# Kernel tuning notes

Measured on AMD Instinct MI355X. Metric: run time of the kernel, lower is better.

The kernel has to match this reference:

```python
import jax, jax.numpy as jnp
import numpy as np

B, S, E, H, L, F = 64, 256, 480, 6, 8, 1920
D = E // H  # 80
VOCAB, MEL, CHORD = 4833, 257, 4833 - 257
EPS = 1e-5


def setup_inputs() -> dict:
    key = jax.random.key(0)
    ks = jax.random.split(key, 24)
    mel = jax.random.randint(ks[0], (B, S), 0, MEL)
    chd = MEL + jax.random.randint(ks[1], (B, S), 0, CHORD)
    pos = jnp.arange(S) % 2  # 0=melody, 1=chord
    input_tokens = jnp.where(pos[None, :] == 1, chd, mel)
    std = 0.02
    n = lambda k, shp: std * jax.random.normal(k, shp, dtype=jnp.float32)
    return {
        'input_tokens': input_tokens,
        'tok_emb': n(ks[2], (VOCAB, E)),
        'pos_emb': n(ks[3], (S, E)),
        'Wq': n(ks[4], (L, E, E)), 'bq': jnp.zeros((L, E)),
        'Wk': n(ks[5], (L, E, E)), 'bk': jnp.zeros((L, E)),
        'Wv': n(ks[6], (L, E, E)), 'bv': jnp.zeros((L, E)),
        'Wo': n(ks[7], (L, E, E)), 'bo': jnp.zeros((L, E)),
        'ln1_s': jnp.ones((L, E)), 'ln1_b': jnp.zeros((L, E)),
        'ln2_s': jnp.ones((L, E)), 'ln2_b': jnp.zeros((L, E)),
        'W1': n(ks[8], (L, F, E)), 'b1': jnp.zeros((L, F)),
        'W2': n(ks[9], (L, E, F)), 'b2': jnp.zeros((L, E)),
        'Wh': n(ks[10], (CHORD, E)), 'bh': jnp.zeros((CHORD,)),
    }


def _ln(x, s, b):
    mu = jnp.mean(x, -1, keepdims=True)
    var = jnp.var(x, -1, keepdims=True)
    return (x - mu) * jax.lax.rsqrt(var + EPS) * s + b


def reference(input_tokens, tok_emb, pos_emb, Wq, bq, Wk, bk, Wv, bv, Wo, bo,
              ln1_s, ln1_b, ln2_s, ln2_b, W1, b1, W2, b2, Wh, bh):
    x = tok_emb[input_tokens] + pos_emb[None, :, :]  # [B,S,E]
    causal = jnp.tril(jnp.ones((S, S), dtype=bool))  # True = keep
    scale = 1.0 / jnp.sqrt(jnp.float32(D))
    for i in range(L):
        h = _ln(x, ln1_s[i], ln1_b[i])
        q = (h @ Wq[i].T + bq[i]).reshape(B, S, H, D).transpose(0, 2, 1, 3)
        k = (h @ Wk[i].T + bk[i]).reshape(B, S, H, D).transpose(0, 2, 1, 3)
        v = (h @ Wv[i].T + bv[i]).reshape(B, S, H, D).transpose(0, 2, 1, 3)
        scores = jnp.einsum('bhsd,bhtd->bhst', q, k) * scale
        scores = jnp.where(causal[None, None], scores, -jnp.inf)
        attn = jax.nn.softmax(scores, axis=-1)
        o = jnp.einsum('bhst,bhtd->bhsd', attn, v)
        o = o.transpose(0, 2, 1, 3).reshape(B, S, E)
        x = x + (o @ Wo[i].T + bo[i])
        h2 = _ln(x, ln2_s[i], ln2_b[i])
        ff = jax.nn.gelu(h2 @ W1[i].T + b1[i], approximate=False) @ W2[i].T + b2[i]
        x = x + ff
    chord = x[:, 1::2, :]  # [B, S//2, E]
    return chord @ Wh.T + bh
```

## Files before the change

kernel.cpp:

```cpp
#include <hip/hip_runtime.h>
#include <hip/hip_bf16.h>
#include <math.h>

#define B_ 64
#define S_ 256
#define E_ 480
#define H_ 6
#define D_ 80
#define L_ 8
#define F_ 1920
#define CHORD_ 4576
#define TOKENS_ (B_*S_)
#define CROWS_ (B_*128)

typedef unsigned short u16;
typedef unsigned int u32;
typedef unsigned long long u64;
typedef __attribute__((ext_vector_type(8))) short short8;
typedef __attribute__((ext_vector_type(4))) float f32x4;
typedef __attribute__((ext_vector_type(4))) u32 u32x4;

__device__ __forceinline__ float bf_lo(u32 u){ return __uint_as_float(u << 16); }
__device__ __forceinline__ float bf_hi(u32 u){ return __uint_as_float(u & 0xffff0000u); }
__device__ __forceinline__ u16 f2bf(float f){
  u32 u = __float_as_uint(f);
  return (u16)((u + 0x7fffu + ((u >> 16) & 1u)) >> 16);
}

__device__ __forceinline__ void async_cp16(void* lds, const void* g){
  __builtin_amdgcn_global_load_lds((const __attribute__((address_space(1))) void*)g,
                                   (__attribute__((address_space(3))) void*)lds, 16, 0, 0);
}

__global__ void cvt_kernel(const float* __restrict__ s, u16* __restrict__ d, int n4)
{
  int i = blockIdx.x * 256 + threadIdx.x;
  const int stride = gridDim.x * 256;
  for (; i < n4; i += stride){
    float4 v = ((const float4*)s)[i];
    u64 w = (u64)((u32)f2bf(v.x) | ((u32)f2bf(v.y) << 16))
          | ((u64)((u32)f2bf(v.z) | ((u32)f2bf(v.w) << 16)) << 32);
    ((u64*)d)[i] = w;
  }
}

__global__ void embed_kernel(const int* __restrict__ tok,
                             const float* __restrict__ tok_emb,
                             const float* __restrict__ pos_emb,
                             float* __restrict__ x)
{
  int row = blockIdx.x;
  int s = row & (S_-1);
  int t = tok[row];
  const float* te = tok_emb + (size_t)t * E_;
  const float* pe = pos_emb + (size_t)s * E_;
  float* xr = x + (size_t)row * E_;
  for (int e = threadIdx.x; e < E_; e += blockDim.x)
    xr[e] = te[e] + pe[e];
}

__global__ __launch_bounds__(256) void ln_kernel(const float* __restrict__ x,
    const float* __restrict__ g, const float* __restrict__ b, u16* __restrict__ o)
{
  int wid = threadIdx.x >> 6, lane = threadIdx.x & 63;
  int row = blockIdx.x * 4 + wid;
  const float* xr = x + (size_t)row * E_;
  float v[8];
  #pragma unroll
  for (int i = 0; i < 7; ++i) v[i] = xr[lane + i*64];
  v[7] = (lane < 32) ? xr[448 + lane] : 0.f;
  float sum = 0.f, sq = 0.f;
  #pragma unroll
  for (int i = 0; i < 8; ++i){ sum += v[i]; sq += v[i]*v[i]; }
  #pragma unroll
  for (int m = 1; m < 64; m <<= 1){ sum += __shfl_xor(sum, m); sq += __shfl_xor(sq, m); }
  float mean = sum * (1.f/E_);
  float var  = sq  * (1.f/E_) - mean*mean;
  float rs = rsqrtf(var + 1e-5f);
  u16* orow = o + (size_t)row * E_;
  #pragma unroll
  for (int i = 0; i < 7; ++i){
    int idx = lane + i*64;
    orow[idx] = f2bf((v[i]-mean)*rs*g[idx] + b[idx]);
  }
  if (lane < 32){
    int idx = 448 + lane;
    orow[idx] = f2bf((v[7]-mean)*rs*g[idx] + b[idx]);
  }
}

template<int MODE>
__global__ __launch_bounds__(256, 4) void gemm_bf_kernel(const u16* __restrict__ A,
                            const u16* __restrict__ Wb, const float* __restrict__ bias,
                            u16* __restrict__ Cb, float* __restrict__ Cf,
                            int M, int N, int K)
{
  __shared__ u16 As[2][128*32];
  __shared__ u16 Ws[2][128*32];
  const int tid = threadIdx.x;
  const int wid = tid >> 6, lane = tid & 63;
  const int wr = wid >> 1, wc = wid & 1;
  const int lr = lane & 15, kg = lane >> 4;
  const int kgs = kg ^ (lr & 3);
  const int m0 = blockIdx.y * 128;
  const int n0 = blockIdx.x * 128;

  const f32x4 zero = {0.f,0.f,0.f,0.f};
  f32x4 acc[4][4];
  #pragma unroll
  for (int i=0;i<4;i++)
    #pragma unroll
    for (int j=0;j<4;j++)
      acc[i][j] = zero;

  const int srow = tid >> 2;
  const int schunk = (tid & 3) ^ (srow & 3);
  const u16* ap0 = A + (size_t)(m0 + srow) * K + schunk*8;
  const u16* ap1 = ap0 + (size_t)64 * K;
  int r0 = n0 + srow, r1 = r0 + 64;
  if (r0 >= N) r0 = N-1;
  if (r1 >= N) r1 = N-1;
  const u16* wp0 = Wb + (size_t)r0 * K + schunk*8;
  const u16* wp1 = Wb + (size_t)r1 * K + schunk*8;

  #define STAGE(bb, k0) do { \
    char* ab = (char*)As[bb] + wid*1024; \
    char* wb_ = (char*)Ws[bb] + wid*1024; \
    async_cp16(ab,        ap0 + (k0)); \
    async_cp16(ab + 4096, ap1 + (k0)); \
    async_cp16(wb_,        wp0 + (k0)); \
    async_cp16(wb_ + 4096, wp1 + (k0)); \
  } while(0)

  const int nsteps = K >> 5;
  STAGE(0, 0);
  __syncthreads();
  int cur = 0;
  for (int ks = 0; ks < nsteps; ++ks){
    if (ks + 1 < nsteps) STAGE(cur^1, (ks+1) << 5);

    short8 af[4], wf[4];
    #pragma unroll
    for (int i=0;i<4;i++) af[i] = *(const short8*)&As[cur][(wr*64 + i*16 + lr)*32 + kgs*8];
    #pragma unroll
    for (int j=0;j<4;j++) wf[j] = *(const short8*)&Ws[cur][(wc*64 + j*16 + lr)*32 + kgs*8];
    #pragma unroll
    for (int i=0;i<4;i++)
      #pragma unroll
      for (int j=0;j<4;j++)
        acc[i][j] = __builtin_amdgcn_mfma_f32_16x16x32_bf16(af[i], wf[j], acc[i][j], 0, 0, 0);

    __syncthreads();
    cur ^= 1;
  }
  #undef STAGE

  #pragma unroll
  for (int i=0;i<4;i++){
    const int row = m0 + wr*64 + i*16 + kg*4;
    #pragma unroll
    for (int j=0;j<4;j++){
      const int col = n0 + wc*64 + j*16 + lr;
      if (col < N){
        const float bv = bias[col];
        #pragma unroll
        for (int q=0;q<4;q++){
          float val = acc[i][j][q] + bv;
          size_t off = (size_t)(row + q) * N + col;
          if (MODE == 0){
            Cb[off] = f2bf(val);
          } else if (MODE == 1){
            float gx = 0.5f * val * (1.f + erff(val * 0.70710678118654752f));
            Cb[off] = f2bf(gx);
          } else if (MODE == 2){
            Cf[off] += val;
          } else {
            Cf[off] = val;
          }
        }
      }
    }
  }
}

template<int MODE>
__global__ __launch_bounds__(256) void gemm_kernel(const u16* __restrict__ A, const float* __restrict__ W,
                            const float* __restrict__ bias,
                            u16* __restrict__ Cb, float* __restrict__ Cf,
                            int M, int N, int K)
{
  __shared__ u16 As[128*32];
  __shared__ u16 Ws[128*32];
  const int tid = threadIdx.x;
  const int wid = tid >> 6, lane = tid & 63;
  const int wr = wid >> 1, wc = wid & 1;
  const int lr = lane & 15, kg = lane >> 4;
  const int m0 = blockIdx.y * 128;
  const int n0 = blockIdx.x * 128;

  const f32x4 zero = {0.f,0.f,0.f,0.f};
  f32x4 acc[4][4];
  #pragma unroll
  for (int i=0;i<4;i++)
    #pragma unroll
    for (int j=0;j<4;j++)
      acc[i][j] = zero;

  const int trow = tid >> 1;
  const int tcol = (tid & 1) * 16;
  const int wn = n0 + trow;
  const bool wok = wn < N;
  const float* wp = W + (size_t)wn * K + tcol;

  const u16* ap0 = A + (size_t)(m0 + (tid>>2)) * K + (tid&3)*8;
  const u16* ap1 = ap0 + (size_t)64 * K;
  char* lb0 = (char*)As + wid*1024;
  char* lb1 = (char*)As + 4096 + wid*1024;
  u32* wdst = (u32*)&Ws[trow*32 + tcol];

  const int nsteps = K >> 5;
  for (int ks = 0; ks < nsteps; ++ks){
    const int k0 = ks << 5;
    async_cp16(lb0, ap0 + k0);
    async_cp16(lb1, ap1 + k0);

    float wv[16];
    if (wok){
      const float4* s4 = (const float4*)(wp + k0);
      #pragma unroll
      for (int i=0;i<4;i++){
        float4 t4 = s4[i];
        wv[4*i]=t4.x; wv[4*i+1]=t4.y; wv[4*i+2]=t4.z; wv[4*i+3]=t4.w;
      }
    } else {
      #pragma unroll
      for (int i=0;i<16;i++) wv[i]=0.f;
    }
    u32 pk[8];
    #pragma unroll
    for (int i=0;i<8;i++) pk[i] = (u32)f2bf(wv[2*i]) | ((u32)f2bf(wv[2*i+1]) << 16);
    #pragma unroll
    for (int i=0;i<8;i++) wdst[i] = pk[i];

    __syncthreads();

    short8 af[4], wf[4];
    #pragma unroll
    for (int i=0;i<4;i++) af[i] = *(const short8*)&As[(wr*64 + i*16 + lr)*32 + kg*8];
    #pragma unroll
    for (int j=0;j<4;j++) wf[j] = *(const short8*)&Ws[(wc*64 + j*16 + lr)*32 + kg*8];
    #pragma unroll
    for (int i=0;i<4;i++)
      #pragma unroll
      for (int j=0;j<4;j++)
        acc[i][j] = __builtin_amdgcn_mfma_f32_16x16x32_bf16(af[i], wf[j], acc[i][j], 0, 0, 0);

    __syncthreads();
  }

  #pragma unroll
  for (int i=0;i<4;i++){
    const int row = m0 + wr*64 + i*16 + kg*4;
    #pragma unroll
    for (int j=0;j<4;j++){
      const int col = n0 + wc*64 + j*16 + lr;
      if (col < N){
        const float bv = bias[col];
        #pragma unroll
        for (int q=0;q<4;q++){
          float val = acc[i][j][q] + bv;
          size_t off = (size_t)(row + q) * N + col;
          if (MODE == 0){
            Cb[off] = f2bf(val);
          } else if (MODE == 1){
            float gx = 0.5f * val * (1.f + erff(val * 0.70710678118654752f));
            Cb[off] = f2bf(gx);
          } else if (MODE == 2){
            Cf[off] += val;
          } else {
            Cf[off] = val;
          }
        }
      }
    }
  }
}

#define KSTRIDE 104
#define VSTRIDE 264
__global__ __launch_bounds__(256) void attn_mfma_kernel(const u16* __restrict__ Q,
    const u16* __restrict__ K, const u16* __restrict__ V, u16* __restrict__ O)
{
  __shared__ u16 ks[256*KSTRIDE];
  __shared__ u16 vt[80*VSTRIDE];
  const int bh = blockIdx.x;
  const int b = bh / H_, h = bh - b*H_;
  const int tid = threadIdx.x;
  const int wv = tid >> 6, lane = tid & 63;
  const int q16 = lane & 15, g = lane >> 4;
  const size_t base = (size_t)b * S_ * E_ + h * D_;

  {
    const uint4* kr = (const uint4*)(K + base + (size_t)tid * E_);
    uint4 t0[10];
    #pragma unroll
    for (int i=0;i<10;i++) t0[i] = kr[i];
    u16* krow = &ks[tid*KSTRIDE];
    #pragma unroll
    for (int i=0;i<10;i++) *(uint4*)&krow[i*8] = t0[i];
    const uint4 z4 = {0,0,0,0};
    *(uint4*)&krow[80] = z4;
    *(uint4*)&krow[88] = z4;
  }
  {
    const u32* vr = (const u32*)(V + base + (size_t)tid * E_);
    u32 t1[40];
    #pragma unroll
    for (int i=0;i<40;i++) t1[i] = vr[i];
    #pragma unroll
    for (int i=0;i<40;i++){
      vt[(2*i)*VSTRIDE + tid]   = (u16)(t1[i] & 0xffffu);
      vt[(2*i+1)*VSTRIDE + tid] = (u16)(t1[i] >> 16);
    }
  }
  short8 bq[4][3];
  const short8 z8 = {0,0,0,0,0,0,0,0};
  #pragma unroll
  for (int i=0;i<4;i++){
    const int qr = 16*wv + 64*i;
    const u16* qrow = Q + (size_t)(b*S_ + qr + q16) * E_ + h*D_;
    bq[i][0] = *(const short8*)&qrow[g*8];
    bq[i][1] = *(const short8*)&qrow[32 + g*8];
    bq[i][2] = (g < 2) ? *(const short8*)&qrow[64 + g*8] : z8;
  }
  __syncthreads();

  f32x4 o_[4][5];
  float m_[4], l_[4];
  #pragma unroll
  for (int i=0;i<4;i++){
    m_[i] = -1e30f; l_[i] = 0.f;
    #pragma unroll
    for (int j=0;j<5;j++) o_[i][j] = (f32x4){0.f,0.f,0.f,0.f};
  }
  const float scale = 0.1118033988749895f;
  const int ktmaxw = (16*wv + 207) >> 5;

  for (int kt = 0; kt <= ktmaxw; ++kt){
    short8 af[2][3];
    #pragma unroll
    for (int a=0;a<2;a++)
      #pragma unroll
      for (int kk=0;kk<3;kk++)
        af[a][kk] = *(const short8*)&ks[(32*kt + 16*a + q16)*KSTRIDE + kk*32 + g*8];
    short8 bvv[5];
    #pragma unroll
    for (int j=0;j<5;j++)
      bvv[j] = *(const short8*)&vt[(16*j + q16)*VSTRIDE + kt*32 + g*8];

    #pragma unroll
    for (int i=0;i<4;i++){
      const int qr = 16*wv + 64*i;
      if (kt > ((qr + 15) >> 5)) continue;
      f32x4 c0 = {0.f,0.f,0.f,0.f}, c1 = {0.f,0.f,0.f,0.f};
      #pragma unroll
      for (int kk=0;kk<3;kk++){
        c0 = __builtin_amdgcn_mfma_f32_16x16x32_bf16(af[0][kk], bq[i][kk], c0, 0, 0, 0);
        c1 = __builtin_amdgcn_mfma_f32_16x16x32_bf16(af[1][kk], bq[i][kk], c1, 0, 0, 0);
      }
      const int qglob = qr + q16;
      const int kb0 = 32*kt + 4*g;
      const bool diag = (32*kt + 31) > qr;
      float s0[4], s1[4];
      #pragma unroll
      for (int r=0;r<4;r++){
        s0[r] = c0[r] * scale;
        s1[r] = c1[r] * scale;
        if (diag){
          if (kb0 + r > qglob)      s0[r] = -3e38f;
          if (kb0 + 16 + r > qglob) s1[r] = -3e38f;
        }
      }
      float mx = fmaxf(fmaxf(fmaxf(s0[0],s0[1]),fmaxf(s0[2],s0[3])),
                       fmaxf(fmaxf(s1[0],s1[1]),fmaxf(s1[2],s1[3])));
      mx = fmaxf(mx, __shfl_xor(mx, 16));
      mx = fmaxf(mx, __shfl_xor(mx, 32));
      const float mnew = fmaxf(m_[i], mx);
      const float resc = __expf(m_[i] - mnew);
      float p0[4], p1[4], ps = 0.f;
      #pragma unroll
      for (int r=0;r<4;r++){
        p0[r] = __expf(s0[r] - mnew);
        p1[r] = __expf(s1[r] - mnew);
        ps += p0[r] + p1[r];
      }
      ps += __shfl_xor(ps, 16);
      ps += __shfl_xor(ps, 32);
      l_[i] = l_[i] * resc + ps;
      m_[i] = mnew;
      float fr[4];
      #pragma unroll
      for (int r=0;r<4;r++) fr[r] = __shfl(resc, 4*g + r);
      #pragma unroll
      for (int j=0;j<5;j++){
        #pragma unroll
        for (int r=0;r<4;r++) o_[i][j][r] *= fr[r];
      }
      u32 pw0 = (u32)f2bf(p0[0]) | ((u32)f2bf(p0[1]) << 16);
      u32 pw1 = (u32)f2bf(p0[2]) | ((u32)f2bf(p0[3]) << 16);
      u32 pw2 = (u32)f2bf(p1[0]) | ((u32)f2bf(p1[1]) << 16);
      u32 pw3 = (u32)f2bf(p1[2]) | ((u32)f2bf(p1[3]) << 16);
      const int s01 = ((((g<<1)&3)<<4) + q16) << 2;
      const int s23 = (((((g<<1)+1)&3)<<4) + q16) << 2;
      int rA0 = __builtin_amdgcn_ds_bpermute(s01, (int)pw0);
      int rB0 = __builtin_amdgcn_ds_bpermute(s01, (int)pw2);
      int rA1 = __builtin_amdgcn_ds_bpermute(s01, (int)pw1);
      int rB1 = __builtin_amdgcn_ds_bpermute(s01, (int)pw3);
      int rA2 = __builtin_amdgcn_ds_bpermute(s23, (int)pw0);
      int rB2 = __builtin_amdgcn_ds_bpermute(s23, (int)pw2);
      int rA3 = __builtin_amdgcn_ds_bpermute(s23, (int)pw1);
      int rB3 = __builtin_amdgcn_ds_bpermute(s23, (int)pw3);
      const bool lo = (g < 2);
      u32x4 rw = { (u32)(lo ? rA0 : rB0), (u32)(lo ? rA1 : rB1),
                   (u32)(lo ? rA2 : rB2), (u32)(lo ? rA3 : rB3) };
      short8 pa = __builtin_bit_cast(short8, rw);
      #pragma unroll
      for (int j=0;j<5;j++)
        o_[i][j] = __builtin_amdgcn_mfma_f32_16x16x32_bf16(pa, bvv[j], o_[i][j], 0, 0, 0);
    }
  }

  #pragma unroll
  for (int i=0;i<4;i++){
    const int qr = 16*wv + 64*i;
    const float inv = 1.f / l_[i];
    float fr[4];
    #pragma unroll
    for (int r=0;r<4;r++) fr[r] = __shfl(inv, 4*g + r);
    #pragma unroll
    for (int j=0;j<5;j++){
      #pragma unroll
      for (int r=0;r<4;r++){
        const int row = qr + 4*g + r;
        O[(size_t)(b*S_ + row) * E_ + h*D_ + 16*j + q16] = f2bf(o_[i][j][r] * fr[r]);
      }
    }
  }
}

__global__ void gather_kernel(const float* __restrict__ x, u16* __restrict__ cin)
{
  int i = blockIdx.x * 256 + threadIdx.x;
  if (i >= CROWS_*E_) return;
  int row = i / E_, col = i - row*E_;
  int b = row >> 7, r = row & 127;
  cin[i] = f2bf(x[((size_t)(b*S_ + 2*r + 1))*E_ + col]);
}

extern "C" void kernel_launch(void* const* d_in, const int* in_sizes, int n_in,
                              void* d_out, int out_size, void* d_ws, size_t ws_size,
                              hipStream_t stream)
{
  (void)in_sizes; (void)n_in; (void)out_size;
  const int*   tok     = (const int*)d_in[0];
  const float* tok_emb = (const float*)d_in[1];
  const float* pos_emb = (const float*)d_in[2];
  const float* Wq = (const float*)d_in[3];
  const float* bq = (const float*)d_in[4];
  const float* Wk = (const float*)d_in[5];
  const float* bk = (const float*)d_in[6];
  const float* Wv = (const float*)d_in[7];
  const float* bv = (const float*)d_in[8];
  const float* Wo = (const float*)d_in[9];
  const float* bo = (const float*)d_in[10];
  const float* ln1s = (const float*)d_in[11];
  const float* ln1b = (const float*)d_in[12];
  const float* ln2s = (const float*)d_in[13];
  const float* ln2b = (const float*)d_in[14];
  const float* W1 = (const float*)d_in[15];
  const float* b1 = (const float*)d_in[16];
  const float* W2 = (const float*)d_in[17];
  const float* b2 = (const float*)d_in[18];
  const float* Wh = (const float*)d_in[19];
  const float* bh = (const float*)d_in[20];

  char* p = (char*)d_ws;
  float* x  = (float*)p;            p += (size_t)TOKENS_*E_*4;
  u16* h    = (u16*)p;              p += (size_t)TOKENS_*E_*2;
  u16* qb   = (u16*)p;
  u16* kb   = qb + (size_t)TOKENS_*E_;
  u16* vb   = kb + (size_t)TOKENS_*E_;
  u16* ao   = vb + (size_t)TOKENS_*E_;
  u16* ff1  = qb;
  u16* cin  = h;
  p += (size_t)4*TOKENS_*E_*2;

  const size_t szE  = (size_t)L_*E_*E_;
  const size_t szF  = (size_t)L_*F_*E_;
  const size_t szH  = (size_t)CHORD_*E_;
  u16* wq_bf = (u16*)p;
  u16* wk_bf = wq_bf + szE;
  u16* wv_bf = wk_bf + szE;
  u16* wo_bf = wv_bf + szE;
  u16* w1_bf = wo_bf + szE;
  u16* w2_bf = w1_bf + szF;
  u16* wh_bf = w2_bf + szF;
  const size_t need = (size_t)110100480 + 2*(4*szE + 2*szF + szH);
  const bool bf16w = (ws_size >= need);

  embed_kernel<<<TOKENS_, 128, 0, stream>>>(tok, tok_emb, pos_emb, x);

  dim3 blk(256);
  dim3 gE(4, TOKENS_/128);
  dim3 gF1(15, TOKENS_/128);
  dim3 gHd(36, CROWS_/128);

  if (bf16w){
    cvt_kernel<<<1024, blk, 0, stream>>>(Wq, wq_bf, (int)(szE/4));
    cvt_kernel<<<1024, blk, 0, stream>>>(Wk, wk_bf, (int)(szE/4));
    cvt_kernel<<<1024, blk, 0, stream>>>(Wv, wv_bf, (int)(szE/4));
    cvt_kernel<<<1024, blk, 0, stream>>>(Wo, wo_bf, (int)(szE/4));
    cvt_kernel<<<1024, blk, 0, stream>>>(W1, w1_bf, (int)(szF/4));
    cvt_kernel<<<1024, blk, 0, stream>>>(W2, w2_bf, (int)(szF/4));
    cvt_kernel<<<1024, blk, 0, stream>>>(Wh, wh_bf, (int)(szH/4));
    for (int i = 0; i < L_; ++i){
      ln_kernel<<<TOKENS_/4, blk, 0, stream>>>(x, ln1s + i*E_, ln1b + i*E_, h);
      gemm_bf_kernel<0><<<gE, blk, 0, stream>>>(h, wq_bf + (size_t)i*E_*E_, bq + i*E_, qb, nullptr, TOKENS_, E_, E_);
      gemm_bf_kernel<0><<<gE, blk, 0, stream>>>(h, wk_bf + (size_t)i*E_*E_, bk + i*E_, kb, nullptr, TOKENS_, E_, E_);
      gemm_bf_kernel<0><<<gE, blk, 0, stream>>>(h, wv_bf + (size_t)i*E_*E_, bv + i*E_, vb, nullptr, TOKENS_, E_, E_);
      attn_mfma_kernel<<<B_*H_, blk, 0, stream>>>(qb, kb, vb, ao);
      gemm_bf_kernel<2><<<gE, blk, 0, stream>>>(ao, wo_bf + (size_t)i*E_*E_, bo + i*E_, nullptr, x, TOKENS_, E_, E_);
      ln_kernel<<<TOKENS_/4, blk, 0, stream>>>(x, ln2s + i*E_, ln2b + i*E_, h);
      gemm_bf_kernel<1><<<gF1, blk, 0, stream>>>(h, w1_bf + (size_t)i*F_*E_, b1 + i*F_, ff1, nullptr, TOKENS_, F_, E_);
      gemm_bf_kernel<2><<<gE, blk, 0, stream>>>(ff1, w2_bf + (size_t)i*E_*F_, b2 + i*E_, nullptr, x, TOKENS_, E_, F_);
    }
    gather_kernel<<<(CROWS_*E_ + 255)/256, blk, 0, stream>>>(x, cin);
    gemm_bf_kernel<3><<<gHd, blk, 0, stream>>>(cin, wh_bf, bh, nullptr, (float*)d_out, CROWS_, CHORD_, E_);
  } else {
    for (int i = 0; i < L_; ++i){
      ln_kernel<<<TOKENS_/4, blk, 0, stream>>>(x, ln1s + i*E_, ln1b + i*E_, h);
      gemm_kernel<0><<<gE, blk, 0, stream>>>(h, Wq + (size_t)i*E_*E_, bq + i*E_, qb, nullptr, TOKENS_, E_, E_);
      gemm_kernel<0><<<gE, blk, 0, stream>>>(h, Wk + (size_t)i*E_*E_, bk + i*E_, kb, nullptr, TOKENS_, E_, E_);
      gemm_kernel<0><<<gE, blk, 0, stream>>>(h, Wv + (size_t)i*E_*E_, bv + i*E_, vb, nullptr, TOKENS_, E_, E_);
      attn_mfma_kernel<<<B_*H_, blk, 0, stream>>>(qb, kb, vb, ao);
      gemm_kernel<2><<<gE, blk, 0, stream>>>(ao, Wo + (size_t)i*E_*E_, bo + i*E_, nullptr, x, TOKENS_, E_, E_);
      ln_kernel<<<TOKENS_/4, blk, 0, stream>>>(x, ln2s + i*E_, ln2b + i*E_, h);
      gemm_kernel<1><<<gF1, blk, 0, stream>>>(h, W1 + (size_t)i*F_*E_, b1 + i*F_, ff1, nullptr, TOKENS_, F_, E_);
      gemm_kernel<2><<<gE, blk, 0, stream>>>(ff1, W2 + (size_t)i*E_*F_, b2 + i*E_, nullptr, x, TOKENS_, E_, F_);
    }
    gather_kernel<<<(CROWS_*E_ + 255)/256, blk, 0, stream>>>(x, cin);
    gemm_kernel<3><<<gHd, blk, 0, stream>>>(cin, Wh, bh, nullptr, (float*)d_out, CROWS_, CHORD_, E_);
  }
}
```

Baseline: 2.412 ms.

## Fuse Q/K/V projections into one GEMM and add XCD-aware tile remapping

```diff
diff --git a/kernel.cpp b/kernel.cpp
--- a/kernel.cpp
+++ b/kernel.cpp
@@ -12,6 +12,7 @@
 #define CHORD_ 4576
 #define TOKENS_ (B_*S_)
 #define CROWS_ (B_*128)
+#define QS_ 1440
 
 typedef unsigned short u16;
 typedef unsigned int u32;
@@ -20,8 +21,6 @@
 typedef __attribute__((ext_vector_type(4))) float f32x4;
 typedef __attribute__((ext_vector_type(4))) u32 u32x4;
 
-__device__ __forceinline__ float bf_lo(u32 u){ return __uint_as_float(u << 16); }
-__device__ __forceinline__ float bf_hi(u32 u){ return __uint_as_float(u & 0xffff0000u); }
 __device__ __forceinline__ u16 f2bf(float f){
   u32 u = __float_as_uint(f);
   return (u16)((u + 0x7fffu + ((u >> 16) & 1u)) >> 16);
@@ -30,6 +29,16 @@
 __device__ __forceinline__ void async_cp16(void* lds, const void* g){
   __builtin_amdgcn_global_load_lds((const __attribute__((address_space(1))) void*)g,
                                    (__attribute__((address_space(3))) void*)lds, 16, 0, 0);
+}
+
+__device__ __forceinline__ void xcd_tile(int gx, int gy, int& tx, int& ty){
+  const int nwg = gx * gy;
+  const int bid = blockIdx.y * gx + blockIdx.x;
+  const int xcd = bid & 7, slot = bid >> 3;
+  const int q8 = nwg >> 3, r8 = nwg & 7;
+  const int t = slot + (xcd < r8 ? xcd * (q8 + 1) : r8 * (q8 + 1) + (xcd - r8) * q8);
+  ty = t / gx;
+  tx = t - ty * gx;
 }
 
 __global__ void cvt_kernel(const float* __restrict__ s, u16* __restrict__ d, int n4)
@@ -42,6 +51,36 @@
           | ((u64)((u32)f2bf(v.z) | ((u32)f2bf(v.w) << 16)) << 32);
     ((u64*)d)[i] = w;
   }
+}
+
+__global__ void qkv_cvt_kernel(const float* __restrict__ Wq, const float* __restrict__ Wk,
+                               const float* __restrict__ Wv, u16* __restrict__ dst)
+{
+  const int per = E_*E_/4;
+  const int tot = L_*3*per;
+  int i = blockIdx.x * 256 + threadIdx.x;
+  const int stride = gridDim.x * 256;
+  for (; i < tot; i += stride){
+    int l = i / (3*per);
+    int rem = i - l*3*per;
+    int sel = rem / per;
+    int r2 = rem - sel*per;
+    const float* src = (sel == 0) ? Wq : (sel == 1) ? Wk : Wv;
+    float4 v = ((const float4*)(src + (size_t)l*E_*E_))[r2];
+    u64 w = (u64)((u32)f2bf(v.x) | ((u32)f2bf(v.y) << 16))
+          | ((u64)((u32)f2bf(v.z) | ((u32)f2bf(v.w) << 16)) << 32);
+    ((u64*)dst)[i] = w;
+  }
+}
+
+__global__ void bias_cat_kernel(const float* __restrict__ bq, const float* __restrict__ bk,
+                                const float* __restrict__ bv, float* __restrict__ dst)
+{
+  int i = blockIdx.x * 256 + threadIdx.x;
+  if (i >= L_*QS_) return;
+  int l = i / QS_, c = i - l*QS_;
+  float v = (c < 480) ? bq[l*480 + c] : (c < 960) ? bk[l*480 + c - 480] : bv[l*480 + c - 960];
+  dst[i] = v;
 }
 
 __global__ void embed_kernel(const int* __restrict__ tok,
@@ -93,7 +132,7 @@
 __global__ __launch_bounds__(256, 4) void gemm_bf_kernel(const u16* __restrict__ A,
                             const u16* __restrict__ Wb, const float* __restrict__ bias,
                             u16* __restrict__ Cb, float* __restrict__ Cf,
-                            int M, int N, int K)
+                            int M, int N, int K, int ldc)
 {
   __shared__ u16 As[2][128*32];
   __shared__ u16 Ws[2][128*32];
@@ -102,8 +141,10 @@
   const int wr = wid >> 1, wc = wid & 1;
   const int lr = lane & 15, kg = lane >> 4;
   const int kgs = kg ^ (lr & 3);
-  const int m0 = blockIdx.y * 128;
-  const int n0 = blockIdx.x * 128;
+  int tx, ty;
+  xcd_tile(gridDim.x, gridDim.y, tx, ty);
+  const int m0 = ty * 128;
+  const int n0 = tx * 128;
 
   const f32x4 zero = {0.f,0.f,0.f,0.f};
   f32x4 acc[4][4];
@@ -166,7 +207,7 @@
         #pragma unroll
         for (int q=0;q<4;q++){
           float val = acc[i][j][q] + bv;
-          size_t off = (size_t)(row + q) * N + col;
+          size_t off = (size_t)(row + q) * ldc + col;
           if (MODE == 0){
             Cb[off] = f2bf(val);
           } else if (MODE == 1){
@@ -187,7 +228,7 @@
 __global__ __launch_bounds__(256) void gemm_kernel(const u16* __restrict__ A, const float* __restrict__ W,
                             const float* __restrict__ bias,
                             u16* __restrict__ Cb, float* __restrict__ Cf,
-                            int M, int N, int K)
+                            int M, int N, int K, int ldc)
 {
   __shared__ u16 As[128*32];
   __shared__ u16 Ws[128*32];
@@ -195,8 +236,10 @@
   const int wid = tid >> 6, lane = tid & 63;
   const int wr = wid >> 1, wc = wid & 1;
   const int lr = lane & 15, kg = lane >> 4;
-  const int m0 = blockIdx.y * 128;
-  const int n0 = blockIdx.x * 128;
+  int tx, ty;
+  xcd_tile(gridDim.x, gridDim.y, tx, ty);
+  const int m0 = ty * 128;
+  const int n0 = tx * 128;
 
   const f32x4 zero = {0.f,0.f,0.f,0.f};
   f32x4 acc[4][4];
@@ -269,7 +312,7 @@
         #pragma unroll
         for (int q=0;q<4;q++){
           float val = acc[i][j][q] + bv;
-          size_t off = (size_t)(row + q) * N + col;
+          size_t off = (size_t)(row + q) * ldc + col;
           if (MODE == 0){
             Cb[off] = f2bf(val);
           } else if (MODE == 1){
@@ -288,8 +331,8 @@
 
 #define KSTRIDE 104
 #define VSTRIDE 264
-__global__ __launch_bounds__(256) void attn_mfma_kernel(const u16* __restrict__ Q,
-    const u16* __restrict__ K, const u16* __restrict__ V, u16* __restrict__ O)
+__global__ __launch_bounds__(256) void attn_mfma_kernel(const u16* __restrict__ QKV,
+                                                        u16* __restrict__ O)
 {
   __shared__ u16 ks[256*KSTRIDE];
   __shared__ u16 vt[80*VSTRIDE];
@@ -298,10 +341,10 @@
   const int tid = threadIdx.x;
   const int wv = tid >> 6, lane = tid & 63;
   const int q16 = lane & 15, g = lane >> 4;
-  const size_t base = (size_t)b * S_ * E_ + h * D_;
+  const size_t rowbase = (size_t)(b*S_ + tid) * QS_ + h * D_;
 
   {
-    const uint4* kr = (const uint4*)(K + base + (size_t)tid * E_);
+    const uint4* kr = (const uint4*)(QKV + rowbase + 480);
     uint4 t0[10];
     #pragma unroll
     for (int i=0;i<10;i++) t0[i] = kr[i];
@@ -313,7 +356,7 @@
     *(uint4*)&krow[88] = z4;
   }
   {
-    const u32* vr = (const u32*)(V + base + (size_t)tid * E_);
+    const u32* vr = (const u32*)(QKV + rowbase + 960);
     u32 t1[40];
     #pragma unroll
     for (int i=0;i<40;i++) t1[i] = vr[i];
@@ -328,7 +371,7 @@
   #pragma unroll
   for (int i=0;i<4;i++){
     const int qr = 16*wv + 64*i;
-    const u16* qrow = Q + (size_t)(b*S_ + qr + q16) * E_ + h*D_;
+    const u16* qrow = QKV + (size_t)(b*S_ + qr + q16) * QS_ + h*D_;
     bq[i][0] = *(const short8*)&qrow[g*8];
     bq[i][1] = *(const short8*)&qrow[32 + g*8];
     bq[i][2] = (g < 2) ? *(const short8*)&qrow[64 + g*8] : z8;
@@ -487,68 +530,63 @@
   char* p = (char*)d_ws;
   float* x  = (float*)p;            p += (size_t)TOKENS_*E_*4;
   u16* h    = (u16*)p;              p += (size_t)TOKENS_*E_*2;
-  u16* qb   = (u16*)p;
-  u16* kb   = qb + (size_t)TOKENS_*E_;
-  u16* vb   = kb + (size_t)TOKENS_*E_;
-  u16* ao   = vb + (size_t)TOKENS_*E_;
-  u16* ff1  = qb;
+  u16* qkv  = (u16*)p;
+  u16* ao   = qkv + (size_t)TOKENS_*QS_;
+  u16* ff1  = qkv;
   u16* cin  = h;
-  p += (size_t)4*TOKENS_*E_*2;
+  p += (size_t)TOKENS_*QS_*2 + (size_t)TOKENS_*E_*2;
 
   const size_t szE  = (size_t)L_*E_*E_;
   const size_t szF  = (size_t)L_*F_*E_;
   const size_t szH  = (size_t)CHORD_*E_;
-  u16* wq_bf = (u16*)p;
-  u16* wk_bf = wq_bf + szE;
-  u16* wv_bf = wk_bf + szE;
-  u16* wo_bf = wv_bf + szE;
-  u16* w1_bf = wo_bf + szE;
-  u16* w2_bf = w1_bf + szF;
-  u16* wh_bf = w2_bf + szF;
-  const size_t need = (size_t)110100480 + 2*(4*szE + 2*szF + szH);
+  u16* wqkv_bf = (u16*)p;            p += 3*szE*2;
+  u16* wo_bf   = (u16*)p;            p += szE*2;
+  u16* w1_bf   = (u16*)p;            p += szF*2;
+  u16* w2_bf   = (u16*)p;            p += szF*2;
+  u16* wh_bf   = (u16*)p;            p += szH*2;
+  float* bqkv  = (float*)p;          p += (size_t)L_*QS_*4;
+  const size_t need = (size_t)(p - (char*)d_ws);
   const bool bf16w = (ws_size >= need);
 
   embed_kernel<<<TOKENS_, 128, 0, stream>>>(tok, tok_emb, pos_emb, x);
 
   dim3 blk(256);
+  dim3 gQKV(12, TOKENS_/128);
   dim3 gE(4, TOKENS_/128);
   dim3 gF1(15, TOKENS_/128);
   dim3 gHd(36, CROWS_/128);
 
   if (bf16w){
-    cvt_kernel<<<1024, blk, 0, stream>>>(Wq, wq_bf, (int)(szE/4));
-    cvt_kernel<<<1024, blk, 0, stream>>>(Wk, wk_bf, (int)(szE/4));
-    cvt_kernel<<<1024, blk, 0, stream>>>(Wv, wv_bf, (int)(szE/4));
+    qkv_cvt_kernel<<<2048, blk, 0, stream>>>(Wq, Wk, Wv, wqkv_bf);
+    bias_cat_kernel<<<(L_*QS_ + 255)/256, blk, 0, stream>>>(bq, bk, bv, bqkv);
     cvt_kernel<<<1024, blk, 0, stream>>>(Wo, wo_bf, (int)(szE/4));
     cvt_kernel<<<1024, blk, 0, stream>>>(W1, w1_bf, (int)(szF/4));
     cvt_kernel<<<1024, blk, 0, stream>>>(W2, w2_bf, (int)(szF/4));
     cvt_kernel<<<1024, blk, 0, stream>>>(Wh, wh_bf, (int)(szH/4));
     for (int i = 0; i < L_; ++i){
       ln_kernel<<<TOKENS_/4, blk, 0, stream>>>(x, ln1s + i*E_, ln1b + i*E_, h);
-      gemm_bf_kernel<0><<<gE, blk, 0, stream>>>(h, wq_bf + (size_t)i*E_*E_, bq + i*E_, qb, nullptr, TOKENS_, E_, E_);
-      gemm_bf_kernel<0><<<gE, blk, 0, stream>>>(h, wk_bf + (size_t)i*E_*E_, bk + i*E_, kb, nullptr, TOKENS_, E_, E_);
-      gemm_bf_kernel<0><<<gE, blk, 0, stream>>>(h, wv_bf + (size_t)i*E_*E_, bv + i*E_, vb, nullptr, TOKENS_, E_, E_);
-      attn_mfma_kernel<<<B_*H_, blk, 0, stream>>>(qb, kb, vb, ao);
-      gemm_bf_kernel<2><<<gE, blk, 0, stream>>>(ao, wo_bf + (size_t)i*E_*E_, bo + i*E_, nullptr, x, TOKENS_, E_, E_);
+      gemm_bf_kernel<0><<<gQKV, blk, 0, stream>>>(h, wqkv_bf + (size_t)i*3*E_*E_, bqkv + i*QS_, qkv, nullptr, TOKENS_, QS_, E_, QS_);
+      attn_mfma_kernel<<<B_*H_, blk, 0, stream>>>(qkv, ao);
+      gemm_bf_kernel<2><<<gE, blk, 0, stream>>>(ao, wo_bf + (size_t)i*E_*E_, bo + i*E_, nullptr, x, TOKENS_, E_, E_, E_);
       ln_kernel<<<TOKENS_/4, blk, 0, stream>>>(x, ln2s + i*E_, ln2b + i*E_, h);
-      gemm_bf_kernel<1><<<gF1, blk, 0, stream>>>(h, w1_bf + (size_t)i*F_*E_, b1 + i*F_, ff1, nullptr, TOKENS_, F_, E_);
-      gemm_bf_kernel<2><<<gE, blk, 0, stream>>>(ff1, w2_bf + (size_t)i*E_*F_, b2 + i*E_, nullptr, x, TOKENS_, E_, F_);
+      gemm_bf_kernel<1><<<gF1, blk, 0, stream>>>(h, w1_bf + (size_t)i*F_*E_, b1 + i*F_, ff1, nullptr, TOKENS_, F_, E_, F_);
+      gemm_bf_kernel<2><<<gE, blk, 0, stream>>>(ff1, w2_bf + (size_t)i*E_*F_, b2 + i*E_, nullptr, x, TOKENS_, E_, F_, E_);
     }
     gather_kernel<<<(CROWS_*E_ + 255)/256, blk, 0, stream>>>(x, cin);
-    gemm_bf_kernel<3><<<gHd, blk, 0, stream>>>(cin, wh_bf, bh, nullptr, (float*)d_out, CROWS_, CHORD_, E_);
+    gemm_bf_kernel<3><<<gHd, blk, 0, stream>>>(cin, wh_bf, bh, nullptr, (float*)d_out, CROWS_, CHORD_, E_, CHORD_);
   } else {
     for (int i = 0; i < L_; ++i){
       ln_kernel<<<TOKENS_/4, blk, 0, stream>>>(x, ln1s + i*E_, ln1b + i*E_, h);
-      gemm_kernel<0><<<gE, blk, 0, stream>>>(h, Wq + (size_t)i*E_*E_, bq + i*E_, qb, nullptr, TOKENS_, E_, E_);
-      gemm_kernel<0><<<gE, blk, 0, stream>>>(h, Wk + (size_t)i*E_*E_, bk + i*E_, kb, nullptr, TOKENS_, E_, E_);
-      gemm_kernel<0><<<gE, blk, 0, stream>>>(h, Wv + (size_t)i*E_*E_, bv + i*E_, vb, nullptr, TOKENS_, E_, E_);
-      attn_mfma_kernel<<<B_*H_, blk, 0, stream>>>(qb, kb, vb, ao);
-      gemm_kernel<2><<<gE, blk, 0, stream>>>(ao, Wo + (size_t)i*E_*E_, bo + i*E_, nullptr, x, TOKENS_, E_, E_);
+      gemm_kernel<0><<<gE, blk, 0, stream>>>(h, Wq + (size_t)i*E_*E_, bq + i*E_, qkv, nullptr, TOKENS_, E_, E_, QS_);
+      gemm_kernel<0><<<gE, blk, 0, stream>>>(h, Wk + (size_t)i*E_*E_, bk + i*E_, qkv + 480, nullptr, TOKENS_, E_, E_, QS_);
+      gemm_kernel<0><<<gE, blk, 0, stream>>>(h, Wv + (size_t)i*E_*E_, bv + i*E_, qkv + 960, nullptr, TOKENS_, E_, E_, QS_);
+      attn_mfma_kernel<<<B_*H_, blk, 0, stream>>>(qkv, ao);
+      gemm_kernel<2><<<gE, blk, 0, stream>>>(ao, Wo + (size_t)i*E_*E_, bo + i*E_, nullptr, x, TOKENS_, E_, E_, E_);
       ln_kernel<<<TOKENS_/4, blk, 0, stream>>>(x, ln2s + i*E_, ln2b + i*E_, h);
-      gemm_kernel<1><<<gF1, blk, 0, stream>>>(h, W1 + (size_t)i*F_*E_, b1 + i*F_, ff1, nullptr, TOKENS_, F_, E_);
-      gemm_kernel<2><<<gE, blk, 0, stream>>>(ff1, W2 + (size_t)i*E_*F_, b2 + i*E_, nullptr, x, TOKENS_, E_, F_);
+      gemm_kernel<1><<<gF1, blk, 0, stream>>>(h, W1 + (size_t)i*F_*E_, b1 + i*F_, ff1, nullptr, TOKENS_, F_, E_, F_);
+      gemm_kernel<2><<<gE, blk, 0, stream>>>(ff1, W2 + (size_t)i*E_*F_, b2 + i*E_, nullptr, x, TOKENS_, E_, F_, E_);
     }
     gather_kernel<<<(CROWS_*E_ + 255)/256, blk, 0, stream>>>(x, cin);
-    gemm_kernel<3><<<gHd, blk, 0, stream>>>(cin, Wh, bh, nullptr, (float*)d_out, CROWS_, CHORD_, E_);
-  }
-}
+    gemm_kernel<3><<<gHd, blk, 0, stream>>>(cin, Wh, bh, nullptr, (float*)d_out, CROWS_, CHORD_, E_, CHORD_);
+  }
+}
```

Result: faster. 2.147 ms (-11.0%).
